# Kernel tuning notes

Measured on AMD Instinct MI355X. Metric: run time of the kernel, lower is better.

The kernel has to match this reference:

```python
import jax, jax.numpy as jnp
import numpy as np
from jax.scipy.stats import norm

N_OBJECTS = 100000
N_DIM = 512
ALPHA = 0.05


def setup_inputs() -> dict:
    key = jax.random.key(0)
    k1, k2 = jax.random.split(key)
    q_mu = jax.random.normal(k1, (N_OBJECTS, N_DIM), dtype=jnp.float32)
    # q_var is used as the Normal scale in the original torch code -> keep it positive
    q_var = jax.random.uniform(k2, (N_OBJECTS, N_DIM), dtype=jnp.float32) * 0.9 + 0.1
    return {"q_mu": q_mu, "q_var": q_var}


def reference(q_mu, q_var):
    n_objects = q_mu.shape[0]
    # ecdf_factor = arange(1..n)/n (the torch buffer, in working dtype)
    ecdf = jnp.arange(1, n_objects + 1, dtype=q_mu.dtype) / n_objects
    # p-values: Normal(loc=q_mu, scale=q_var).cdf(0), transposed -> [n_dim, n_objects]
    pvals = norm.cdf(0.0, loc=q_mu, scale=q_var).T

    idx = jnp.arange(n_objects)

    def fdr_reject(p):  # p: [n_objects]
        sortind = jnp.argsort(p)
        ps = p[sortind]
        reject = ps <= ecdf * ALPHA
        # torch code: rejectmax = first nonzero index; reject[:rejectmax] = True
        first = jnp.argmax(reject)
        reject = jnp.where(reject.any(), reject | (idx < first), reject)
        # unsort back to original order (reject_[sortind] = reject)
        return jnp.zeros_like(reject).at[sortind].set(reject)

    rejections = jax.vmap(fdr_reject)(pvals)  # [n_dim, n_objects] bool
    importance = rejections.sum(axis=1)       # [n_dim]
    return importance
```

## Files before the change

### kernel.cpp

```cpp
#include <hip/hip_runtime.h>
#include <cstdint>
#include <cstddef>


#define N_OBJ  100000
#define N_DIM  512
#define UCAP   15360
#define TROW   64
#define TDIM   64

__global__ __launch_bounds__(256) void u_kernel(
    const float* __restrict__ mu, const float* __restrict__ var,
    unsigned short* __restrict__ ut, int c0, int dimTiles)
{
    __shared__ unsigned short tile[TROW][TDIM + 8];
    const int tid = threadIdx.x;
    const int dt = blockIdx.x % dimTiles;
    const int rt = blockIdx.x / dimTiles;
    const int r0 = rt * TROW;
    const int d0 = c0 + dt * TDIM;

    #pragma unroll
    for (int it = 0; it < 4; ++it) {
        const int slot = it * 256 + tid;
        const int rl = slot >> 4;
        const int q  = slot & 15;
        const int r  = r0 + rl;
        ushort4 pk = make_ushort4(0, 0, 0, 0);
        if (r < N_OBJ) {
            const size_t off = (size_t)r * N_DIM + d0 + (q << 2);
            const float4 m4 = *(const float4*)(mu + off);
            const float4 v4 = *(const float4*)(var + off);
            const float xs[4] = {m4.x / v4.x, m4.y / v4.y, m4.z / v4.z, m4.w / v4.w};
            unsigned short us[4];
            #pragma unroll
            for (int j = 0; j < 4; ++j) {
                const float p = 0.5f * erfcf(xs[j] * 0.70710678118654752f);
                const float s = p * 2000000.0f;
                unsigned short u = 0;
                if (s <= (float)UCAP) {
                    const int ui = (int)ceilf(s);
                    u = (unsigned short)(ui < 1 ? 1 : ui);
                }
                us[j] = u;
            }
            pk = make_ushort4(us[0], us[1], us[2], us[3]);
        }
        *(ushort4*)&tile[rl][q << 2] = pk;
    }
    __syncthreads();

    const int d  = tid >> 2;
    const int rb = (tid & 3) << 4;
    union { unsigned short s[16]; uint4 v[2]; } pk;
    #pragma unroll
    for (int i = 0; i < 16; ++i) pk.s[i] = tile[rb + i][d];
    const size_t base = (size_t)(dt * TDIM + d) * N_OBJ + (size_t)(r0 + rb);
    if (r0 + rb + 15 < N_OBJ) {
        *(uint4*)(ut + base)     = pk.v[0];
        *(uint4*)(ut + base + 8) = pk.v[1];
    } else {
        #pragma unroll
        for (int i = 0; i < 16; ++i)
            if (r0 + rb + i < N_OBJ) ut[base + i] = pk.s[i];
    }
}

__global__ __launch_bounds__(256) void fdr_kernel(
    const unsigned short* __restrict__ ut, int* __restrict__ out, int c0)
{
    __shared__ unsigned int hist[UCAP];
    __shared__ unsigned int wsum[4];
    __shared__ unsigned int redc[4], redm[4];
    const int tid  = threadIdx.x;
    const int lane = tid & 63;
    const int wid  = tid >> 6;
    const unsigned short* __restrict__ row = ut + (size_t)blockIdx.x * N_OBJ;

    for (int i = tid; i < UCAP / 4; i += 256)
        ((uint4*)hist)[i] = make_uint4(0u, 0u, 0u, 0u);
    __syncthreads();

    unsigned int c1 = 0;
    for (int slot = tid; slot < N_OBJ / 8; slot += 256) {
        const uint4 w = *(const uint4*)(row + slot * 8);
        const unsigned int words[4] = {w.x, w.y, w.z, w.w};
        #pragma unroll
        for (int k = 0; k < 4; ++k) {
            const unsigned int u0 = words[k] & 0xFFFFu;
            const unsigned int u1 = words[k] >> 16;
            if (u0 == 1u) c1++; else if (u0) atomicAdd(&hist[u0 - 1], 1u);
            if (u1 == 1u) c1++; else if (u1) atomicAdd(&hist[u1 - 1], 1u);
        }
    }
    #pragma unroll
    for (int d = 32; d > 0; d >>= 1) c1 += __shfl_down(c1, d, 64);
    if (lane == 0 && c1) atomicAdd(&hist[0], c1);
    __syncthreads();

    unsigned int running = 0, tcount = 0, tmin = 0xFFFFFFFFu;
    for (int u0 = 0; u0 < UCAP; u0 += 1024) {
        const int idx = u0 + (tid << 2);
        const uint4 c = *(const uint4*)&hist[idx];
        const unsigned int ls = c.x + c.y + c.z + c.w;

        unsigned int sc = ls;
        #pragma unroll
        for (int dd = 1; dd < 64; dd <<= 1) {
            const unsigned int v = __shfl_up(sc, dd, 64);
            if (lane >= dd) sc += v;
        }
        if (lane == 63) wsum[wid] = sc;
        __syncthreads();

        unsigned int woff = 0, btot = 0;
        #pragma unroll
        for (int w = 0; w < 4; ++w) {
            const unsigned int s = wsum[w];
            btot += s;
            if (w < wid) woff += s;
        }

        unsigned int P = running + woff + (sc - ls);
        const unsigned int cc[4] = {c.x, c.y, c.z, c.w};
        #pragma unroll
        for (int j = 0; j < 4; ++j) {
            P += cc[j];
            const unsigned int m = (unsigned int)(idx + j + 1);
            if (P >= m) { tcount++; if (m < tmin) tmin = m; }
        }
        running += btot;
        __syncthreads();
    }

    #pragma unroll
    for (int d = 32; d > 0; d >>= 1) {
        tcount += __shfl_down(tcount, d, 64);
        const unsigned int om = __shfl_down(tmin, d, 64);
        if (om < tmin) tmin = om;
    }
    if (lane == 0) { redc[wid] = tcount; redm[wid] = tmin; }
    __syncthreads();
    if (tid == 0) {
        const unsigned int tot = redc[0] + redc[1] + redc[2] + redc[3];
        const unsigned int mn  = min(min(redm[0], redm[1]), min(redm[2], redm[3]));
        out[c0 + blockIdx.x] = tot ? (int)(tot + mn - 1u) : 0;
    }
}

extern "C" void kernel_launch(void* const* d_in, const int* in_sizes, int n_in,
                              void* d_out, int out_size, void* d_ws, size_t ws_size,
                              hipStream_t stream) {
    const float* mu  = (const float*)d_in[0];
    const float* var = (const float*)d_in[1];
    int* out = (int*)d_out;
    unsigned short* ut = (unsigned short*)d_ws;

    const size_t perDim = (size_t)N_OBJ * sizeof(unsigned short);
    const int dmax = (int)(ws_size / perDim);
    int D_c = N_DIM;
    while (D_c > dmax && D_c > TDIM) D_c >>= 1;

    const int rowTiles = (N_OBJ + TROW - 1) / TROW;
    for (int c0 = 0; c0 < N_DIM; c0 += D_c) {
        const int dimTiles = D_c / TDIM;
        u_kernel<<<rowTiles * dimTiles, 256, 0, stream>>>(mu, var, ut, c0, dimTiles);
        fdr_kernel<<<D_c, 256, 0, stream>>>(ut, out, c0);
    }
}
```

Before: 475.8 us.

## Fuse p-value computation into global-atomic histograms, dropping the transposed u16 buffer

```diff
diff --git a/kernel.cpp b/kernel.cpp
--- a/kernel.cpp
+++ b/kernel.cpp
@@ -6,109 +6,75 @@
 #define N_OBJ  100000
 #define N_DIM  512
 #define UCAP   15360
-#define TROW   64
-#define TDIM   64
 
-__global__ __launch_bounds__(256) void u_kernel(
+__global__ __launch_bounds__(256) void zero_kernel(uint4* __restrict__ p, int n4)
+{
+    const int i = blockIdx.x * 256 + threadIdx.x;
+    if (i < n4) p[i] = make_uint4(0u, 0u, 0u, 0u);
+}
+
+__global__ __launch_bounds__(256) void u_hist_kernel(
     const float* __restrict__ mu, const float* __restrict__ var,
-    unsigned short* __restrict__ ut, int c0, int dimTiles)
+    unsigned int* __restrict__ hist, int c0, int dc, int nslots)
 {
-    __shared__ unsigned short tile[TROW][TDIM + 8];
-    const int tid = threadIdx.x;
-    const int dt = blockIdx.x % dimTiles;
-    const int rt = blockIdx.x / dimTiles;
-    const int r0 = rt * TROW;
-    const int d0 = c0 + dt * TDIM;
+    const int slot = blockIdx.x * 256 + threadIdx.x;
+    if (slot >= nslots) return;
+    const int qpr = dc >> 2;
+    const int r   = slot / qpr;
+    const int dl  = (slot - r * qpr) << 2;
+    const size_t off = (size_t)r * N_DIM + c0 + dl;
+    const float4 m4 = *(const float4*)(mu + off);
+    const float4 v4 = *(const float4*)(var + off);
+    const float ms[4] = {m4.x, m4.y, m4.z, m4.w};
+    const float vs[4] = {v4.x, v4.y, v4.z, v4.w};
 
     #pragma unroll
-    for (int it = 0; it < 4; ++it) {
-        const int slot = it * 256 + tid;
-        const int rl = slot >> 4;
-        const int q  = slot & 15;
-        const int r  = r0 + rl;
-        ushort4 pk = make_ushort4(0, 0, 0, 0);
-        if (r < N_OBJ) {
-            const size_t off = (size_t)r * N_DIM + d0 + (q << 2);
-            const float4 m4 = *(const float4*)(mu + off);
-            const float4 v4 = *(const float4*)(var + off);
-            const float xs[4] = {m4.x / v4.x, m4.y / v4.y, m4.z / v4.z, m4.w / v4.w};
-            unsigned short us[4];
-            #pragma unroll
-            for (int j = 0; j < 4; ++j) {
-                const float p = 0.5f * erfcf(xs[j] * 0.70710678118654752f);
-                const float s = p * 2000000.0f;
-                unsigned short u = 0;
-                if (s <= (float)UCAP) {
-                    const int ui = (int)ceilf(s);
-                    u = (unsigned short)(ui < 1 ? 1 : ui);
-                }
-                us[j] = u;
+    for (int j = 0; j < 4; ++j) {
+        const float m = ms[j], v = vs[j];
+        if (m < 2.0f * v) continue;
+        unsigned int u;
+        if (m > 6.0f * v) {
+            u = 1u;
+        } else {
+            const float x = m / v;
+            const float p = 0.5f * erfcf(x * 0.70710678118654752f);
+            const float s = p * 2000000.0f;
+            if (s <= (float)UCAP) {
+                const int ui = (int)ceilf(s);
+                u = (unsigned int)(ui < 1 ? 1 : ui);
+            } else {
+                u = 0u;
             }
-            pk = make_ushort4(us[0], us[1], us[2], us[3]);
         }
-        *(ushort4*)&tile[rl][q << 2] = pk;
-    }
-    __syncthreads();
-
-    const int d  = tid >> 2;
-    const int rb = (tid & 3) << 4;
-    union { unsigned short s[16]; uint4 v[2]; } pk;
-    #pragma unroll
-    for (int i = 0; i < 16; ++i) pk.s[i] = tile[rb + i][d];
-    const size_t base = (size_t)(dt * TDIM + d) * N_OBJ + (size_t)(r0 + rb);
-    if (r0 + rb + 15 < N_OBJ) {
-        *(uint4*)(ut + base)     = pk.v[0];
-        *(uint4*)(ut + base + 8) = pk.v[1];
-    } else {
-        #pragma unroll
-        for (int i = 0; i < 16; ++i)
-            if (r0 + rb + i < N_OBJ) ut[base + i] = pk.s[i];
+        if (u) atomicAdd(&hist[(size_t)(dl + j) * UCAP + (u - 1u)], 1u);
     }
 }
 
-__global__ __launch_bounds__(256) void fdr_kernel(
-    const unsigned short* __restrict__ ut, int* __restrict__ out, int c0)
+__global__ __launch_bounds__(256) void scan_kernel(
+    const unsigned int* __restrict__ hist, int* __restrict__ out, int c0)
 {
-    __shared__ unsigned int hist[UCAP];
     __shared__ unsigned int wsum[4];
     __shared__ unsigned int redc[4], redm[4];
     const int tid  = threadIdx.x;
     const int lane = tid & 63;
     const int wid  = tid >> 6;
-    const unsigned short* __restrict__ row = ut + (size_t)blockIdx.x * N_OBJ;
-
-    for (int i = tid; i < UCAP / 4; i += 256)
-        ((uint4*)hist)[i] = make_uint4(0u, 0u, 0u, 0u);
-    __syncthreads();
-
-    unsigned int c1 = 0;
-    for (int slot = tid; slot < N_OBJ / 8; slot += 256) {
-        const uint4 w = *(const uint4*)(row + slot * 8);
-        const unsigned int words[4] = {w.x, w.y, w.z, w.w};
-        #pragma unroll
-        for (int k = 0; k < 4; ++k) {
-            const unsigned int u0 = words[k] & 0xFFFFu;
-            const unsigned int u1 = words[k] >> 16;
-            if (u0 == 1u) c1++; else if (u0) atomicAdd(&hist[u0 - 1], 1u);
-            if (u1 == 1u) c1++; else if (u1) atomicAdd(&hist[u1 - 1], 1u);
-        }
-    }
-    #pragma unroll
-    for (int d = 32; d > 0; d >>= 1) c1 += __shfl_down(c1, d, 64);
-    if (lane == 0 && c1) atomicAdd(&hist[0], c1);
-    __syncthreads();
+    const unsigned int* __restrict__ h = hist + (size_t)blockIdx.x * UCAP;
 
     unsigned int running = 0, tcount = 0, tmin = 0xFFFFFFFFu;
+    uint4 c = *(const uint4*)&h[tid << 2];
     for (int u0 = 0; u0 < UCAP; u0 += 1024) {
+        uint4 cn = make_uint4(0u, 0u, 0u, 0u);
+        const int nidx = u0 + 1024 + (tid << 2);
+        if (nidx < UCAP) cn = *(const uint4*)&h[nidx];
+
         const int idx = u0 + (tid << 2);
-        const uint4 c = *(const uint4*)&hist[idx];
         const unsigned int ls = c.x + c.y + c.z + c.w;
 
         unsigned int sc = ls;
         #pragma unroll
         for (int dd = 1; dd < 64; dd <<= 1) {
-            const unsigned int v = __shfl_up(sc, dd, 64);
-            if (lane >= dd) sc += v;
+            const unsigned int vv = __shfl_up(sc, dd, 64);
+            if (lane >= dd) sc += vv;
         }
         if (lane == 63) wsum[wid] = sc;
         __syncthreads();
@@ -126,11 +92,12 @@
         #pragma unroll
         for (int j = 0; j < 4; ++j) {
             P += cc[j];
-            const unsigned int m = (unsigned int)(idx + j + 1);
-            if (P >= m) { tcount++; if (m < tmin) tmin = m; }
+            const unsigned int mm = (unsigned int)(idx + j + 1);
+            if (P >= mm) { tcount++; if (mm < tmin) tmin = mm; }
         }
         running += btot;
         __syncthreads();
+        c = cn;
     }
 
     #pragma unroll
@@ -150,21 +117,22 @@
 
 extern "C" void kernel_launch(void* const* d_in, const int* in_sizes, int n_in,
                               void* d_out, int out_size, void* d_ws, size_t ws_size,
-                              hipStream_t stream) {
+                              hipStream_t stream)
+{
     const float* mu  = (const float*)d_in[0];
     const float* var = (const float*)d_in[1];
     int* out = (int*)d_out;
-    unsigned short* ut = (unsigned short*)d_ws;
+    unsigned int* hist = (unsigned int*)d_ws;
 
-    const size_t perDim = (size_t)N_OBJ * sizeof(unsigned short);
-    const int dmax = (int)(ws_size / perDim);
     int D_c = N_DIM;
-    while (D_c > dmax && D_c > TDIM) D_c >>= 1;
+    while ((size_t)D_c * UCAP * sizeof(unsigned int) > ws_size && D_c > 4) D_c >>= 1;
 
-    const int rowTiles = (N_OBJ + TROW - 1) / TROW;
     for (int c0 = 0; c0 < N_DIM; c0 += D_c) {
-        const int dimTiles = D_c / TDIM;
-        u_kernel<<<rowTiles * dimTiles, 256, 0, stream>>>(mu, var, ut, c0, dimTiles);
-        fdr_kernel<<<D_c, 256, 0, stream>>>(ut, out, c0);
+        const int n4 = D_c * UCAP / 4;
+        zero_kernel<<<(n4 + 255) / 256, 256, 0, stream>>>((uint4*)hist, n4);
+        const int nslots = N_OBJ * (D_c / 4);
+        u_hist_kernel<<<(nslots + 255) / 256, 256, 0, stream>>>(
+            mu, var, hist, c0, D_c, nslots);
+        scan_kernel<<<D_c, 256, 0, stream>>>(hist, out, c0);
     }
 }
```

Result: slower. 634.0 us (+33.3%).
